# Performance work log

Measured on AMD Instinct MI355X. Metric: run time of the kernel, lower is better.

## Reference

```python
import jax, jax.numpy as jnp
import numpy as np

FP8_MAX = 448.0  # torch.finfo(float8_e4m3fn).max


def quant_fp8(x):
    # dynamic per-tensor quantization: amax -> scale -> cast to fp8
    amax = jnp.max(jnp.abs(x)).astype(jnp.float32)
    scale = jnp.minimum(FP8_MAX / jnp.maximum(amax, 1e-12), FP8_MAX)
    x_fp8 = jnp.clip(x * scale, -FP8_MAX, FP8_MAX).astype(jnp.float8_e4m3fn)
    return x_fp8, 1.0 / scale  # (fp8 data, dequant scale)


def setup_inputs() -> dict:
    key = jax.random.key(0)
    k1, k2, k3 = jax.random.split(key, 3)
    B, S, IN, OUT = 4, 8192, 1024, 1024
    input = jax.random.normal(k1, (B, S, IN), dtype=jnp.float32)
    # kaiming_uniform_(a=sqrt(5)) -> uniform(-1/sqrt(in), 1/sqrt(in))
    bound = 1.0 / np.sqrt(IN)
    weight = jax.random.uniform(k2, (OUT, IN), dtype=jnp.float32, minval=-bound, maxval=bound)
    bias = jax.random.uniform(k3, (OUT,), dtype=jnp.float32, minval=-bound, maxval=bound)
    return {"input": input, "weight": weight, "bias": bias}


def reference(input, weight, bias):
    prev_shape = input.shape
    x2d = input.reshape(-1, weight.shape[1])  # [T, in]
    w_fp8, w_scale = quant_fp8(weight)
    x_fp8, x_scale = quant_fp8(x2d)
    # bias add, bf16 output
    acc = jnp.matmul(x_fp8.astype(jnp.float32), w_fp8.astype(jnp.float32).T)
    out2d = (acc * (x_scale * w_scale) + bias).astype(jnp.bfloat16)
    out = out2d.reshape(*prev_shape[:-1], weight.shape[0]).astype(input.dtype)
    return out
```

## Files before the change

kernel.cpp:

```cpp
#include <hip/hip_runtime.h>
#include <hip/hip_bf16.h>

typedef float f32x4 __attribute__((ext_vector_type(4)));
typedef float f32x16 __attribute__((ext_vector_type(16)));
typedef int   i32x4  __attribute__((ext_vector_type(4)));
typedef int   i32x8  __attribute__((ext_vector_type(8)));

#define FP8_MAX_F 448.0f
#define SCL1 0x7F7F7F7Fu

__device__ __forceinline__ float wave_max(float m) {
#pragma unroll
    for (int off = 32; off > 0; off >>= 1)
        m = fmaxf(m, __shfl_xor(m, off));
    return m;
}

__global__ void amax2_kernel(const float* __restrict__ x, long nx,
                             const float* __restrict__ w, long nw,
                             float* __restrict__ px, float* __restrict__ pw,
                             int ga) {
    __shared__ float red[4];
    const float* src; long n; float* dst; int bid, blocks;
    if ((int)blockIdx.x < ga) { src = x; n = nx; dst = px; bid = blockIdx.x; blocks = ga; }
    else { src = w; n = nw; dst = pw; bid = blockIdx.x - ga; blocks = gridDim.x - ga; }

    const long stride = (long)blocks * blockDim.x * 16;
    long i = ((long)bid * blockDim.x + threadIdx.x) * 16;
    float m = 0.0f;
    for (; i < n; i += stride) {
        f32x4 v0 = *(const f32x4*)(src + i);
        f32x4 v1 = *(const f32x4*)(src + i + 4);
        f32x4 v2 = *(const f32x4*)(src + i + 8);
        f32x4 v3 = *(const f32x4*)(src + i + 12);
        float m0 = fmaxf(fmaxf(fabsf(v0.x), fabsf(v0.y)), fmaxf(fabsf(v0.z), fabsf(v0.w)));
        float m1 = fmaxf(fmaxf(fabsf(v1.x), fabsf(v1.y)), fmaxf(fabsf(v1.z), fabsf(v1.w)));
        float m2 = fmaxf(fmaxf(fabsf(v2.x), fabsf(v2.y)), fmaxf(fabsf(v2.z), fabsf(v2.w)));
        float m3 = fmaxf(fmaxf(fabsf(v3.x), fabsf(v3.y)), fmaxf(fabsf(v3.z), fabsf(v3.w)));
        m = fmaxf(m, fmaxf(fmaxf(m0, m1), fmaxf(m2, m3)));
    }
    m = wave_max(m);
    const int wave = threadIdx.x >> 6;
    if ((threadIdx.x & 63) == 0) red[wave] = m;
    __syncthreads();
    if (threadIdx.x == 0)
        dst[bid] = fmaxf(fmaxf(red[0], red[1]), fmaxf(red[2], red[3]));
}

__global__ void amax_final_kernel(const float* __restrict__ px, int npx,
                                  const float* __restrict__ pw, int npw,
                                  unsigned* __restrict__ amax) {
    __shared__ float red[4];
    const float* p; int n;
    if (blockIdx.x == 0) { p = px; n = npx; } else { p = pw; n = npw; }
    float m = 0.0f;
    for (int i = threadIdx.x; i < n; i += blockDim.x) m = fmaxf(m, p[i]);
    m = wave_max(m);
    const int wave = threadIdx.x >> 6;
    if ((threadIdx.x & 63) == 0) red[wave] = m;
    __syncthreads();
    if (threadIdx.x == 0) {
        m = fmaxf(fmaxf(red[0], red[1]), fmaxf(red[2], red[3]));
        amax[blockIdx.x] = __float_as_uint(m);
    }
}

__global__ void quant2_kernel(const float* __restrict__ x, long nx8,
                              const float* __restrict__ w, long nw8,
                              const unsigned* __restrict__ amax_bits,
                              unsigned* __restrict__ qx, unsigned* __restrict__ qw,
                              int ga) {
    const float* src; long n8; unsigned* q; int bid, blocks; float a;
    if ((int)blockIdx.x < ga) { src = x; n8 = nx8; q = qx; bid = blockIdx.x; blocks = ga;
                                a = __uint_as_float(amax_bits[0]); }
    else { src = w; n8 = nw8; q = qw; bid = blockIdx.x - ga; blocks = gridDim.x - ga;
           a = __uint_as_float(amax_bits[1]); }
    const float scale = fminf(FP8_MAX_F / fmaxf(a, 1e-12f), FP8_MAX_F);

    const long stride = (long)blocks * blockDim.x;
    for (long i = (long)bid * blockDim.x + threadIdx.x; i < n8; i += stride) {
        f32x4 v0 = *(const f32x4*)(src + i * 8);
        f32x4 v1 = *(const f32x4*)(src + i * 8 + 4);
        float c0 = fminf(fmaxf(v0.x * scale, -FP8_MAX_F), FP8_MAX_F);
        float c1 = fminf(fmaxf(v0.y * scale, -FP8_MAX_F), FP8_MAX_F);
        float c2 = fminf(fmaxf(v0.z * scale, -FP8_MAX_F), FP8_MAX_F);
        float c3 = fminf(fmaxf(v0.w * scale, -FP8_MAX_F), FP8_MAX_F);
        float c4 = fminf(fmaxf(v1.x * scale, -FP8_MAX_F), FP8_MAX_F);
        float c5 = fminf(fmaxf(v1.y * scale, -FP8_MAX_F), FP8_MAX_F);
        float c6 = fminf(fmaxf(v1.z * scale, -FP8_MAX_F), FP8_MAX_F);
        float c7 = fminf(fmaxf(v1.w * scale, -FP8_MAX_F), FP8_MAX_F);
        int r0 = __builtin_amdgcn_cvt_pk_fp8_f32(c0, c1, 0, false);
        r0 = __builtin_amdgcn_cvt_pk_fp8_f32(c2, c3, r0, true);
        int r1 = __builtin_amdgcn_cvt_pk_fp8_f32(c4, c5, 0, false);
        r1 = __builtin_amdgcn_cvt_pk_fp8_f32(c6, c7, r1, true);
        uint2 rr; rr.x = (unsigned)r0; rr.y = (unsigned)r1;
        *(uint2*)(q + i * 2) = rr;
    }
}

__global__ __launch_bounds__(512, 1) void gemm_fp8_kernel(
    const unsigned char* __restrict__ Xq,
    const unsigned char* __restrict__ Wq,
    const float* __restrict__ bias,
    const unsigned* __restrict__ amax_bits,
    float* __restrict__ out,
    int M, int N, int K, int nbn)
{
    __shared__ unsigned char ldsA[3][16384];
    __shared__ unsigned char ldsB[3][16384];

    const int tid  = threadIdx.x;
    const int lane = tid & 63;
    const int wave = tid >> 6;
    const int wm128 = (wave >> 2) * 128;
    const int wn64  = (wave & 3) * 64;

    const int l31 = lane & 31;
    const int g   = lane >> 5;

    const int cpx = gridDim.x >> 3;
    const int wg  = ((int)blockIdx.x & 7) * cpx + ((int)blockIdx.x >> 3);
    const int bn = wg % nbn;
    const int bm = wg / nbn;
    const int rowStart = bm << 8;
    const int colStart = bn << 8;

    const int aoffL = (2 * g) * 4096 + (wm128 + l31) * 16;
    const int boffL = (2 * g) * 4096 + (wn64  + l31) * 16;

    const size_t aoffs = (size_t)(rowStart + (tid & 255)) * K + (tid >> 8) * 16;
    const size_t boffs = (size_t)(colStart + (tid & 255)) * K + (tid >> 8) * 16;
    const int tid16 = tid * 16;

    union Frag { i32x8 v; struct { i32x4 lo, hi; } h; };
    f32x16 acc[4][2] = {};

#define STAGE_A(t, sl)                                                                          \
    do {                                                                                        \
        const size_t kk_ = (size_t)(t) * 64;                                                    \
        __builtin_amdgcn_global_load_lds(                                                       \
            (const __attribute__((address_space(1))) void*)(Xq + aoffs + kk_),                  \
            (__attribute__((address_space(3))) void*)(&ldsA[sl][tid16]), 16, 0, 0);             \
        __builtin_amdgcn_global_load_lds(                                                       \
            (const __attribute__((address_space(1))) void*)(Xq + aoffs + 32 + kk_),             \
            (__attribute__((address_space(3))) void*)(&ldsA[sl][8192 + tid16]), 16, 0, 0);      \
    } while (0)

#define STAGE_B(t, sl)                                                                          \
    do {                                                                                        \
        const size_t kk_ = (size_t)(t) * 64;                                                    \
        __builtin_amdgcn_global_load_lds(                                                       \
            (const __attribute__((address_space(1))) void*)(Wq + boffs + kk_),                  \
            (__attribute__((address_space(3))) void*)(&ldsB[sl][tid16]), 16, 0, 0);             \
        __builtin_amdgcn_global_load_lds(                                                       \
            (const __attribute__((address_space(1))) void*)(Wq + boffs + 32 + kk_),             \
            (__attribute__((address_space(3))) void*)(&ldsB[sl][8192 + tid16]), 16, 0, 0);      \
    } while (0)

#define RD_FRAGS(sl, FA, FB)                                                                    \
    do {                                                                                        \
        const unsigned char* rA_ = &ldsA[sl][0];                                                \
        const unsigned char* rB_ = &ldsB[sl][0];                                                \
        _Pragma("unroll")                                                                       \
        for (int mt_ = 0; mt_ < 4; ++mt_) {                                                     \
            FA[mt_].h.lo = *(const i32x4*)(rA_ + aoffL + mt_ * 512);                            \
            FA[mt_].h.hi = *(const i32x4*)(rA_ + aoffL + 4096 + mt_ * 512);                     \
        }                                                                                       \
        _Pragma("unroll")                                                                       \
        for (int nt_ = 0; nt_ < 2; ++nt_) {                                                     \
            FB[nt_].h.lo = *(const i32x4*)(rB_ + boffL + nt_ * 512);                            \
            FB[nt_].h.hi = *(const i32x4*)(rB_ + boffL + 4096 + nt_ * 512);                     \
        }                                                                                       \
    } while (0)

#define MFMA8(FA, FB)                                                                           \
    do {                                                                                        \
        __builtin_amdgcn_s_setprio(1);                                                          \
        _Pragma("unroll")                                                                       \
        for (int mt_ = 0; mt_ < 4; ++mt_)                                                       \
            _Pragma("unroll")                                                                   \
            for (int nt_ = 0; nt_ < 2; ++nt_)                                                   \
                acc[mt_][nt_] = __builtin_amdgcn_mfma_scale_f32_32x32x64_f8f6f4(                \
                    FA[mt_].v, FB[nt_].v, acc[mt_][nt_], 0, 0, 0, SCL1, 0, SCL1);               \
        __builtin_amdgcn_s_setprio(0);                                                          \
    } while (0)

#define BODY(t, sNext, sStage, FA, FB, FA2, FB2)                                                \
    do {                                                                                        \
        if ((t) + 2 < nT) { STAGE_A((t) + 2, sStage); STAGE_B((t) + 2, sStage); }               \
        asm volatile("s_waitcnt lgkmcnt(0)" ::: "memory");                                      \
        __builtin_amdgcn_sched_barrier(0);                                                      \
        MFMA8(FA, FB);                                                                          \
        if ((t) + 2 < nT) asm volatile("s_waitcnt vmcnt(4)" ::: "memory");                      \
        else              asm volatile("s_waitcnt vmcnt(0)" ::: "memory");                      \
        __builtin_amdgcn_s_barrier();                                                           \
        __builtin_amdgcn_sched_barrier(0);                                                      \
        if ((t) + 1 < nT) RD_FRAGS(sNext, FA2, FB2);                                            \
    } while (0)

    STAGE_A(0, 0); STAGE_B(0, 0);
    STAGE_A(1, 1); STAGE_B(1, 1);
    asm volatile("s_waitcnt vmcnt(4)" ::: "memory");
    __builtin_amdgcn_s_barrier();
    __builtin_amdgcn_sched_barrier(0);

    Frag faA[4], fbA[2], faB[4], fbB[2];
    RD_FRAGS(0, faA, fbA);

    const int nT = K >> 6;
    int s = 0;
#pragma unroll 1
    for (int t = 0; t < nT; t += 2) {
        const int s1 = (s + 1 >= 3) ? s - 2 : s + 1;
        const int s2 = (s + 2 >= 3) ? s - 1 : s + 2;
        BODY(t,     s1, s2, faA, fbA, faB, fbB);
        BODY(t + 1, s2, s,  faB, fbB, faA, fbA);
        s = s2;
    }
#undef BODY
#undef MFMA8
#undef RD_FRAGS
#undef STAGE_A
#undef STAGE_B

    const float ax = __uint_as_float(amax_bits[0]);
    const float aw = __uint_as_float(amax_bits[1]);
    const float sx = fminf(FP8_MAX_F / fmaxf(ax, 1e-12f), FP8_MAX_F);
    const float sw = fminf(FP8_MAX_F / fmaxf(aw, 1e-12f), FP8_MAX_F);
    const float sc = (1.0f / sx) * (1.0f / sw);

#pragma unroll
    for (int nt = 0; nt < 2; ++nt) {
        const int col = colStart + wn64 + nt * 32 + l31;
        const float bv = bias[col];
#pragma unroll
        for (int mt = 0; mt < 4; ++mt) {
#pragma unroll
            for (int r = 0; r < 16; ++r) {
                const int row = rowStart + wm128 + mt * 32 + (r & 3) + 8 * (r >> 2) + 4 * g;
                float tt = acc[mt][nt][r] * sc;
                tt = tt + bv;
                out[(size_t)row * N + col] = __bfloat162float(__float2bfloat16(tt));
            }
        }
    }
}

extern "C" void kernel_launch(void* const* d_in, const int* in_sizes, int n_in,
                              void* d_out, int out_size, void* d_ws, size_t ws_size,
                              hipStream_t stream) {
    const float* input  = (const float*)d_in[0];
    const float* weight = (const float*)d_in[1];
    const float* bias   = (const float*)d_in[2];
    float* out = (float*)d_out;

    const int K = 1024;
    const int N = in_sizes[2];
    const long nX = in_sizes[0];
    const long nW = (long)N * K;
    const int M = (int)(nX / K);

    const int GA = 1984;
    const int GW = 64;

    unsigned char* ws = (unsigned char*)d_ws;
    unsigned* amax = (unsigned*)ws;
    unsigned char* Xq = ws + 256;
    unsigned char* Wq = Xq + (size_t)M * K;
    float* px = (float*)(Wq + (size_t)N * K);
    float* pw = px + GA;

    amax2_kernel<<<GA + GW, 256, 0, stream>>>(input, nX, weight, nW, px, pw, GA);
    amax_final_kernel<<<2, 256, 0, stream>>>(px, GA, pw, GW, amax);

    quant2_kernel<<<2048, 256, 0, stream>>>(input, nX / 8, weight, nW / 8, amax,
                                            (unsigned*)Xq, (unsigned*)Wq, GA);

    const int nbn = N / 256;
    const int nwg = (M / 256) * nbn;
    gemm_fp8_kernel<<<dim3(nwg), dim3(512), 0, stream>>>(Xq, Wq, bias, amax, out, M, N, K, nbn);
}
```

Before: 119.5 us.

## Switch GEMM mainloop to double-buffered 128-wide K tiles with split staging

The FP8 GEMM main loop moves from a triple-buffered 64-wide K pipeline with register double-buffered fragments to a double-buffered 128-wide K tile. Each iteration waits for all loads, then issues the next tile's A and B loads interleaved with two half-tile fragment reads and MFMA groups. The aim is fewer barriers per unit of K and larger global loads per stage. The cost is a full vmcnt(0) wait at every tile and no register-level prefetch overlap of LDS reads with MFMAs. The loop still assumes nT is even, which holds for K=1024.

Measured after the change: 264.1 us. +121.0%, slower.

```diff
diff --git a/kernel.cpp b/kernel.cpp
--- a/kernel.cpp
+++ b/kernel.cpp
@@ -106,8 +106,8 @@
     float* __restrict__ out,
     int M, int N, int K, int nbn)
 {
-    __shared__ unsigned char ldsA[3][16384];
-    __shared__ unsigned char ldsB[3][16384];
+    __shared__ unsigned char ldsA[2][32768];
+    __shared__ unsigned char ldsB[2][32768];
 
     const int tid  = threadIdx.x;
     const int lane = tid & 63;
@@ -137,43 +137,43 @@
 
 #define STAGE_A(t, sl)                                                                          \
     do {                                                                                        \
-        const size_t kk_ = (size_t)(t) * 64;                                                    \
-        __builtin_amdgcn_global_load_lds(                                                       \
-            (const __attribute__((address_space(1))) void*)(Xq + aoffs + kk_),                  \
-            (__attribute__((address_space(3))) void*)(&ldsA[sl][tid16]), 16, 0, 0);             \
-        __builtin_amdgcn_global_load_lds(                                                       \
-            (const __attribute__((address_space(1))) void*)(Xq + aoffs + 32 + kk_),             \
-            (__attribute__((address_space(3))) void*)(&ldsA[sl][8192 + tid16]), 16, 0, 0);      \
+        const size_t kk_ = (size_t)(t) * 128;                                                   \
+        _Pragma("unroll")                                                                       \
+        for (int c_ = 0; c_ < 4; ++c_)                                                          \
+            __builtin_amdgcn_global_load_lds(                                                   \
+                (const __attribute__((address_space(1))) void*)(Xq + aoffs + kk_ + c_ * 32),    \
+                (__attribute__((address_space(3))) void*)(&ldsA[sl][c_ * 8192 + tid16]),        \
+                16, 0, 0);                                                                      \
     } while (0)
 
 #define STAGE_B(t, sl)                                                                          \
     do {                                                                                        \
-        const size_t kk_ = (size_t)(t) * 64;                                                    \
-        __builtin_amdgcn_global_load_lds(                                                       \
-            (const __attribute__((address_space(1))) void*)(Wq + boffs + kk_),                  \
-            (__attribute__((address_space(3))) void*)(&ldsB[sl][tid16]), 16, 0, 0);             \
-        __builtin_amdgcn_global_load_lds(                                                       \
-            (const __attribute__((address_space(1))) void*)(Wq + boffs + 32 + kk_),             \
-            (__attribute__((address_space(3))) void*)(&ldsB[sl][8192 + tid16]), 16, 0, 0);      \
-    } while (0)
-
-#define RD_FRAGS(sl, FA, FB)                                                                    \
+        const size_t kk_ = (size_t)(t) * 128;                                                   \
+        _Pragma("unroll")                                                                       \
+        for (int c_ = 0; c_ < 4; ++c_)                                                          \
+            __builtin_amdgcn_global_load_lds(                                                   \
+                (const __attribute__((address_space(1))) void*)(Wq + boffs + kk_ + c_ * 32),    \
+                (__attribute__((address_space(3))) void*)(&ldsB[sl][c_ * 8192 + tid16]),        \
+                16, 0, 0);                                                                      \
+    } while (0)
+
+#define RD_KH(kh, sl)                                                                           \
     do {                                                                                        \
         const unsigned char* rA_ = &ldsA[sl][0];                                                \
         const unsigned char* rB_ = &ldsB[sl][0];                                                \
         _Pragma("unroll")                                                                       \
         for (int mt_ = 0; mt_ < 4; ++mt_) {                                                     \
-            FA[mt_].h.lo = *(const i32x4*)(rA_ + aoffL + mt_ * 512);                            \
-            FA[mt_].h.hi = *(const i32x4*)(rA_ + aoffL + 4096 + mt_ * 512);                     \
+            fa[mt_].h.lo = *(const i32x4*)(rA_ + aoffL + (kh) * 16384 + mt_ * 512);             \
+            fa[mt_].h.hi = *(const i32x4*)(rA_ + aoffL + (kh) * 16384 + 4096 + mt_ * 512);      \
         }                                                                                       \
         _Pragma("unroll")                                                                       \
         for (int nt_ = 0; nt_ < 2; ++nt_) {                                                     \
-            FB[nt_].h.lo = *(const i32x4*)(rB_ + boffL + nt_ * 512);                            \
-            FB[nt_].h.hi = *(const i32x4*)(rB_ + boffL + 4096 + nt_ * 512);                     \
+            fb[nt_].h.lo = *(const i32x4*)(rB_ + boffL + (kh) * 16384 + nt_ * 512);             \
+            fb[nt_].h.hi = *(const i32x4*)(rB_ + boffL + (kh) * 16384 + 4096 + nt_ * 512);      \
         }                                                                                       \
     } while (0)
 
-#define MFMA8(FA, FB)                                                                           \
+#define MFMA8()                                                                                 \
     do {                                                                                        \
         __builtin_amdgcn_s_setprio(1);                                                          \
         _Pragma("unroll")                                                                       \
@@ -181,45 +181,39 @@
             _Pragma("unroll")                                                                   \
             for (int nt_ = 0; nt_ < 2; ++nt_)                                                   \
                 acc[mt_][nt_] = __builtin_amdgcn_mfma_scale_f32_32x32x64_f8f6f4(                \
-                    FA[mt_].v, FB[nt_].v, acc[mt_][nt_], 0, 0, 0, SCL1, 0, SCL1);               \
+                    fa[mt_].v, fb[nt_].v, acc[mt_][nt_], 0, 0, 0, SCL1, 0, SCL1);               \
         __builtin_amdgcn_s_setprio(0);                                                          \
     } while (0)
 
-#define BODY(t, sNext, sStage, FA, FB, FA2, FB2)                                                \
-    do {                                                                                        \
-        if ((t) + 2 < nT) { STAGE_A((t) + 2, sStage); STAGE_B((t) + 2, sStage); }               \
+#define BODY(t, s)                                                                              \
+    do {                                                                                        \
+        asm volatile("s_waitcnt vmcnt(0)" ::: "memory");                                        \
+        __builtin_amdgcn_s_barrier();                                                           \
+        __builtin_amdgcn_sched_barrier(0);                                                      \
+        if ((t) + 1 < nT) STAGE_A((t) + 1, (s) ^ 1);                                            \
+        RD_KH(0, s);                                                                            \
         asm volatile("s_waitcnt lgkmcnt(0)" ::: "memory");                                      \
         __builtin_amdgcn_sched_barrier(0);                                                      \
-        MFMA8(FA, FB);                                                                          \
-        if ((t) + 2 < nT) asm volatile("s_waitcnt vmcnt(4)" ::: "memory");                      \
-        else              asm volatile("s_waitcnt vmcnt(0)" ::: "memory");                      \
-        __builtin_amdgcn_s_barrier();                                                           \
+        MFMA8();                                                                                \
+        if ((t) + 1 < nT) STAGE_B((t) + 1, (s) ^ 1);                                            \
+        RD_KH(1, s);                                                                            \
+        asm volatile("s_waitcnt lgkmcnt(0)" ::: "memory");                                      \
         __builtin_amdgcn_sched_barrier(0);                                                      \
-        if ((t) + 1 < nT) RD_FRAGS(sNext, FA2, FB2);                                            \
+        MFMA8();                                                                                \
     } while (0)
 
     STAGE_A(0, 0); STAGE_B(0, 0);
-    STAGE_A(1, 1); STAGE_B(1, 1);
-    asm volatile("s_waitcnt vmcnt(4)" ::: "memory");
-    __builtin_amdgcn_s_barrier();
-    __builtin_amdgcn_sched_barrier(0);
-
-    Frag faA[4], fbA[2], faB[4], fbB[2];
-    RD_FRAGS(0, faA, fbA);
-
-    const int nT = K >> 6;
-    int s = 0;
+
+    Frag fa[4], fb[2];
+    const int nT = K >> 7;
 #pragma unroll 1
     for (int t = 0; t < nT; t += 2) {
-        const int s1 = (s + 1 >= 3) ? s - 2 : s + 1;
-        const int s2 = (s + 2 >= 3) ? s - 1 : s + 2;
-        BODY(t,     s1, s2, faA, fbA, faB, fbB);
-        BODY(t + 1, s2, s,  faB, fbB, faA, fbA);
-        s = s2;
+        BODY(t, 0);
+        BODY(t + 1, 1);
     }
 #undef BODY
 #undef MFMA8
-#undef RD_FRAGS
+#undef RD_KH
 #undef STAGE_A
 #undef STAGE_B
 
```
